# Kernel tuning notes

Hardware: AMD Instinct MI355X
Metric: run time of the kernel (lower is better)

Reference implementation:

```python
import jax, jax.numpy as jnp
import numpy as np

# Mesh hierarchy: V0=20480 -> V1=5120 -> V2=1280 -> V3=320, spiral seq=9, pool nnz/row K=3
B, V0, V1, V2, V3, S, K = 16, 20480, 5120, 1280, 320, 9, 3
CIN, H = 3, (64, 128, 256)
Z = 256


def spiral_conv(x, idx, W, b):
    # x: [B, V_in, C]; idx: [V, S] spiral neighbor indices; W: [S*C, C_out]
    Bx = x.shape[0]
    g = x[:, idx.reshape(-1), :].reshape(Bx, idx.shape[0], -1)  # [B, V, S*C]
    return g @ W + b


def pool(x, idx, w):
    # sparse transform [V_out, V_in] with K nnz per row: idx/w [V_out, K]
    return jnp.einsum('bvkc,vk->bvc', x[:, idx], w)


def setup_inputs() -> dict:
    key = jax.random.key(0)
    ks = iter(jax.random.split(key, 64))

    def nrm(shape, fan_in):
        return jax.random.normal(next(ks), shape, jnp.float32) / np.float32(np.sqrt(fan_in))

    def ridx(shape, hi):
        return jax.random.randint(next(ks), shape, 0, hi, dtype=jnp.int32)

    def pw(shape):
        w = jax.random.uniform(next(ks), shape, jnp.float32)
        return w / jnp.sum(w, axis=-1, keepdims=True)  # row-stochastic pool weights

    inp = {
        'x': jax.random.normal(next(ks), (B, V0, CIN), jnp.float32),
        'enc_W0': nrm((S * CIN, H[0]), S * CIN), 'enc_b0': jnp.zeros((H[0],), jnp.float32),
        'enc_W1': nrm((S * H[0], H[1]), S * H[0]), 'enc_b1': jnp.zeros((H[1],), jnp.float32),
        'enc_W2': nrm((S * H[1], H[2]), S * H[1]), 'enc_b2': jnp.zeros((H[2],), jnp.float32),
        'Wz': nrm((V3 * H[2], Z), V3 * H[2]), 'bz': jnp.zeros((Z,), jnp.float32),
        'Wp': nrm((Z, H[2] * V3), Z), 'bp': jnp.zeros((H[2] * V3,), jnp.float32),
        'dec_W0': nrm((S * H[2], H[1]), S * H[2]), 'dec_b0': jnp.zeros((H[1],), jnp.float32),
        'dec_W1': nrm((S * H[1], H[0]), S * H[1]), 'dec_b1': jnp.zeros((H[0],), jnp.float32),
        'dec_W2': nrm((S * H[0], CIN), S * H[0]), 'dec_b2': jnp.zeros((CIN,), jnp.float32),
        'dpool_w0': pw((V1, K)), 'dpool_w1': pw((V2, K)), 'dpool_w2': pw((V3, K)),
        'upool_w0': pw((V2, K)), 'upool_w1': pw((V1, K)), 'upool_w2': pw((V0, K)),
        'idx0': ridx((V0, S), V0), 'idx1': ridx((V1, S), V1), 'idx2': ridx((V2, S), V2),
        'dpool_idx0': ridx((V1, K), V0), 'dpool_idx1': ridx((V2, K), V1), 'dpool_idx2': ridx((V3, K), V2),
        'upool_idx0': ridx((V2, K), V3), 'upool_idx1': ridx((V1, K), V2), 'upool_idx2': ridx((V0, K), V1),
    }
    return inp


def reference(x, enc_W0, enc_b0, enc_W1, enc_b1, enc_W2, enc_b2, Wz, bz, Wp, bp,
              dec_W0, dec_b0, dec_W1, dec_b1, dec_W2, dec_b2,
              dpool_w0, dpool_w1, dpool_w2, upool_w0, upool_w1, upool_w2,
              idx0, idx1, idx2, dpool_idx0, dpool_idx1, dpool_idx2,
              upool_idx0, upool_idx1, upool_idx2):
    elu = jax.nn.elu
    # ---- encoder: conv -> elu -> down-pool (x3), then flatten -> latent linear
    h = pool(elu(spiral_conv(x, idx0, enc_W0, enc_b0)), dpool_idx0, dpool_w0)   # [B,V1,64]
    h = pool(elu(spiral_conv(h, idx1, enc_W1, enc_b1)), dpool_idx1, dpool_w1)   # [B,V2,128]
    h = pool(elu(spiral_conv(h, idx2, enc_W2, enc_b2)), dpool_idx2, dpool_w2)   # [B,V3,256]
    z = h.reshape(h.shape[0], V3 * H[2]) @ Wz + bz                              # [B,256]
    # ---- decoder: project -> (up-pool -> conv -> act) x3, last act identity
    d = (z @ Wp + bp).reshape(z.shape[0], V3, H[2])                             # [B,V3,256]
    d = elu(spiral_conv(pool(d, upool_idx0, upool_w0), idx2, dec_W0, dec_b0))   # [B,V2,128]
    d = elu(spiral_conv(pool(d, upool_idx1, upool_w1), idx1, dec_W1, dec_b1))   # [B,V1,64]
    y = spiral_conv(pool(d, upool_idx2, upool_w2), idx0, dec_W2, dec_b2)        # [B,V0,3]
    return (y, z)
```

## Files before the change

### kernel.cpp

```cpp
#include <hip/hip_runtime.h>
#include <hip/hip_bf16.h>
#include <math.h>

typedef __hip_bfloat16 bf16;
typedef short bf16x8 __attribute__((ext_vector_type(8)));
typedef float f32x4 __attribute__((ext_vector_type(4)));

__device__ __forceinline__ float bfbits2f(unsigned int u) {
    union { unsigned int i; float f; } c; c.i = u << 16; return c.f;
}
__device__ __forceinline__ float b2f(const bf16 v) {
    return __bfloat162float(v);
}
__device__ __forceinline__ unsigned short f2bbits(float f) {
    unsigned int x = __float_as_uint(f);
    x += 0x7fffu + ((x >> 16) & 1u);
    return (unsigned short)(x >> 16);
}
__device__ __forceinline__ void unpack8(const uint4 v, float* f) {
    f[0]=bfbits2f(v.x & 0xffffu); f[1]=bfbits2f(v.x >> 16);
    f[2]=bfbits2f(v.y & 0xffffu); f[3]=bfbits2f(v.y >> 16);
    f[4]=bfbits2f(v.z & 0xffffu); f[5]=bfbits2f(v.z >> 16);
    f[6]=bfbits2f(v.w & 0xffffu); f[7]=bfbits2f(v.w >> 16);
}
__device__ __forceinline__ float ldx(const float* p) { return *p; }
__device__ __forceinline__ float ldx(const bf16* p)  { return b2f(*p); }

__global__ void zero_k(float* p, int n) {
    int e = blockIdx.x * 256 + threadIdx.x;
    if (e < n) p[e] = 0.f;
}

__global__ void pack_k(const float* __restrict__ W, bf16* __restrict__ o,
                       const int K, const int COUT, const int NT, const int KP32) {
    const int e = blockIdx.x * 256 + threadIdx.x;
    const int total = KP32 * NT * 512;
    if (e >= total) return;
    const int j    = e & 7;
    const int lane = (e >> 3) & 63;
    const int rest = e >> 9;
    const int nt   = rest % NT;
    const int kt2  = rest / NT;
    const int k = kt2 * 32 + ((lane >> 4) << 3) + j;
    const int n = nt * 16 + (lane & 15);
    float v = (k < K && n < COUT) ? W[(size_t)k * COUT + n] : 0.f;
    union { unsigned short u; bf16 h; } c; c.u = f2bbits(v);
    o[e] = c.h;
}

template<typename XT, typename OT, int CIN, int COUT, bool ELU>
__global__ __launch_bounds__(256) void mconv_k(
    const XT* __restrict__ x, const int* __restrict__ idx,
    const bf16* __restrict__ Wpk, const float* __restrict__ bias,
    OT* __restrict__ out, const int V, const int Vin)
{
    constexpr int K    = 9 * CIN;
    constexpr int KC   = (CIN >= 64) ? 64 : 32;
    constexpr int NKC  = (K + KC - 1) / KC;
    constexpr int KS   = KC / 32;
    constexpr int NT   = (COUT + 15) / 16;
    constexpr int ROWB = KC * 2;
    constexpr int SWZ  = (KC == 64) ? 7 : 3;

    __shared__ __align__(16) char alds[2][64 * ROWB];

    const int t  = threadIdx.x;
    const int w  = t >> 6;
    const int l  = t & 63;
    const int r0 = blockIdx.x * 64;
    const int b  = r0 / V;
    const int v0 = r0 - b * V;

    f32x4 acc[NT];
    #pragma unroll
    for (int nt = 0; nt < NT; ++nt) acc[nt] = (f32x4){0.f, 0.f, 0.f, 0.f};

    if constexpr (CIN >= 64) {
        const int srow = t >> 2, u2 = t & 3;
        const int src = idx[(v0 + srow) * 9];
        const XT* gp = x + ((size_t)b * Vin + src) * CIN + u2 * 16;
        const uint4 a0 = *(const uint4*)gp;
        const uint4 a1 = *(const uint4*)(gp + 8);
        char* wb = alds[0] + srow * ROWB;
        const int m = (srow & 7) << 4;
        *(uint4*)(wb + ((u2 * 32) ^ m))      = a0;
        *(uint4*)(wb + ((u2 * 32 + 16) ^ m)) = a1;
    } else {
        for (int e = t; e < 64 * 32; e += 256) {
            const int row = e >> 5, k = e & 31;
            unsigned short hv = 0;
            if (k < K) {
                const int s = k / CIN, ci = k - s * CIN;
                const int src = idx[(v0 + row) * 9 + s];
                hv = f2bbits(ldx(x + ((size_t)b * Vin + src) * CIN + ci));
            }
            const int m2 = (row & 3) << 4;
            *(unsigned short*)(alds[0] + row * 64 + ((k * 2) ^ m2)) = hv;
        }
    }
    __syncthreads();

    const int rl = (w << 4) + (l & 15);
    const int rm = (rl & SWZ) << 4;
    const bf16x8* wpb = (const bf16x8*)Wpk;

    uint4 n0, n1;
    for (int kt = 0; kt < NKC; ++kt) {
        const bool hn = (kt + 1 < NKC);
        if constexpr (CIN >= 64) {
            if (hn) {
                const int srow = t >> 2, u2 = t & 3;
                const int kn = kt + 1;
                const int s   = (kn * 64) / CIN;
                const int ci0 = (kn * 64) - s * CIN;
                const int src = idx[(v0 + srow) * 9 + s];
                const XT* gp = x + ((size_t)b * Vin + src) * CIN + ci0 + u2 * 16;
                n0 = *(const uint4*)gp;
                n1 = *(const uint4*)(gp + 8);
            }
        }
        const char* ab = alds[kt & 1] + rl * ROWB;
        #pragma unroll
        for (int ks = 0; ks < KS; ++ks) {
            union { uint4 u; bf16x8 v; } af;
            af.u = *(const uint4*)(ab + ((ks * 64 + ((l >> 4) << 4)) ^ rm));
            const size_t wbase = ((size_t)(kt * KS + ks) * NT) * 64 + l;
            #pragma unroll
            for (int nt = 0; nt < NT; ++nt) {
                const bf16x8 bfv = wpb[wbase + (size_t)nt * 64];
                acc[nt] = __builtin_amdgcn_mfma_f32_16x16x32_bf16(af.v, bfv, acc[nt], 0, 0, 0);
            }
        }
        if constexpr (CIN >= 64) {
            if (hn) {
                const int srow = t >> 2, u2 = t & 3;
                char* wb = alds[(kt + 1) & 1] + srow * ROWB;
                const int m = (srow & 7) << 4;
                *(uint4*)(wb + ((u2 * 32) ^ m))      = n0;
                *(uint4*)(wb + ((u2 * 32 + 16) ^ m)) = n1;
            }
        }
        __syncthreads();
    }

    const int colg = l & 15;
    const int rg   = (l >> 4) << 2;
    #pragma unroll
    for (int nt = 0; nt < NT; ++nt) {
        const int n = nt * 16 + colg;
        if constexpr (COUT < 16) { if (n >= COUT) continue; }
        const float bv = bias[n];
        #pragma unroll
        for (int rr = 0; rr < 4; ++rr) {
            float a = acc[nt][rr] + bv;
            if constexpr (ELU) a = a > 0.f ? a : (__expf(a) - 1.f);
            const size_t o = (size_t)(r0 + (w << 4) + rg + rr) * COUT + n;
            if constexpr (__is_same(OT, float)) {
                out[o] = a;
            } else {
                union { unsigned short u; bf16 h; } c; c.u = f2bbits(a);
                out[o] = c.h;
            }
        }
    }
}

__global__ __launch_bounds__(256) void pool_k(
    const bf16* __restrict__ in, const int* __restrict__ idx,
    const float* __restrict__ w, bf16* __restrict__ out,
    const int Vout, const int Vin, const int C)
{
    const int nC8 = C >> 3;
    const long long total = (long long)16 * Vout * nC8;
    const long long gid = (long long)blockIdx.x * 256 + threadIdx.x;
    if (gid >= total) return;
    const int c8 = (int)(gid % nC8);
    const long long bv = gid / nC8;
    const int vo = (int)(bv % Vout);
    const int b  = (int)(bv / Vout);

    float r[8];
    #pragma unroll
    for (int u = 0; u < 8; ++u) r[u] = 0.f;
    #pragma unroll
    for (int jj = 0; jj < 3; ++jj) {
        const int src = idx[vo * 3 + jj];
        const float ww = w[vo * 3 + jj];
        const uint4 xv = *(const uint4*)(in + ((size_t)b * Vin + src) * C + c8 * 8);
        float f[8]; unpack8(xv, f);
        #pragma unroll
        for (int u = 0; u < 8; ++u) r[u] += ww * f[u];
    }
    uint4 st;
    st.x = f2bbits(r[0]) | ((unsigned)f2bbits(r[1]) << 16);
    st.y = f2bbits(r[2]) | ((unsigned)f2bbits(r[3]) << 16);
    st.z = f2bbits(r[4]) | ((unsigned)f2bbits(r[5]) << 16);
    st.w = f2bbits(r[6]) | ((unsigned)f2bbits(r[7]) << 16);
    *(uint4*)(out + ((size_t)b * Vout + vo) * C + c8 * 8) = st;
}

__global__ __launch_bounds__(256) void zacc_k(
    const bf16* __restrict__ F, const float* __restrict__ Wz, float* __restrict__ zf)
{
    const int j  = threadIdx.x;
    const int i0 = blockIdx.x * 256;
    float acc[16];
    #pragma unroll
    for (int b = 0; b < 16; ++b) acc[b] = 0.f;
    for (int i = i0; i < i0 + 256; i += 8) {
        float w[8];
        #pragma unroll
        for (int u = 0; u < 8; ++u) w[u] = Wz[(size_t)(i + u) * 256 + j];
        #pragma unroll
        for (int b = 0; b < 16; ++b) {
            const uint4 fv = *(const uint4*)(F + (size_t)b * 81920 + i);
            float f[8]; unpack8(fv, f);
            #pragma unroll
            for (int u = 0; u < 8; ++u) acc[b] += f[u] * w[u];
        }
    }
    #pragma unroll
    for (int b = 0; b < 16; ++b) atomicAdd(&zf[b * 256 + j], acc[b]);
}

__global__ void zfin_k(float* __restrict__ zf, const float* __restrict__ bz,
                       float* __restrict__ outz)
{
    int e = blockIdx.x * 256 + threadIdx.x;
    int j = e & 255;
    float v = zf[e] + bz[j];
    zf[e] = v;
    outz[e] = v;
}

__global__ __launch_bounds__(256) void dproj_k(
    const float* __restrict__ zf, const float* __restrict__ Wp,
    const float* __restrict__ bp, bf16* __restrict__ d)
{
    __shared__ float zl[256][16];
    const int t = threadIdx.x;
    #pragma unroll
    for (int b = 0; b < 16; ++b) zl[t][b] = zf[b * 256 + t];
    __syncthreads();
    const size_t j = (size_t)blockIdx.x * 256 + t;
    const float bpv = bp[j];
    float acc[16];
    #pragma unroll
    for (int b = 0; b < 16; ++b) acc[b] = bpv;
    for (int k = 0; k < 256; ++k) {
        const float w = Wp[(size_t)k * 81920 + j];
        #pragma unroll
        for (int b = 0; b < 16; ++b) acc[b] += zl[k][b] * w;
    }
    #pragma unroll
    for (int b = 0; b < 16; ++b) {
        union { unsigned short u; bf16 h; } c; c.u = f2bbits(acc[b]);
        d[(size_t)b * 81920 + j] = c.h;
    }
}

extern "C" void kernel_launch(void* const* d_in, const int* in_sizes, int n_in,
                              void* d_out, int out_size, void* d_ws, size_t ws_size,
                              hipStream_t stream) {
    (void)in_sizes; (void)n_in; (void)out_size; (void)ws_size;
    const float* x     = (const float*)d_in[0];
    const float* encW0 = (const float*)d_in[1];
    const float* encb0 = (const float*)d_in[2];
    const float* encW1 = (const float*)d_in[3];
    const float* encb1 = (const float*)d_in[4];
    const float* encW2 = (const float*)d_in[5];
    const float* encb2 = (const float*)d_in[6];
    const float* Wz    = (const float*)d_in[7];
    const float* bz    = (const float*)d_in[8];
    const float* Wp    = (const float*)d_in[9];
    const float* bp    = (const float*)d_in[10];
    const float* decW0 = (const float*)d_in[11];
    const float* decb0 = (const float*)d_in[12];
    const float* decW1 = (const float*)d_in[13];
    const float* decb1 = (const float*)d_in[14];
    const float* decW2 = (const float*)d_in[15];
    const float* decb2 = (const float*)d_in[16];
    const float* dpw0  = (const float*)d_in[17];
    const float* dpw1  = (const float*)d_in[18];
    const float* dpw2  = (const float*)d_in[19];
    const float* upw0  = (const float*)d_in[20];
    const float* upw1  = (const float*)d_in[21];
    const float* upw2  = (const float*)d_in[22];
    const int* idx0    = (const int*)d_in[23];
    const int* idx1    = (const int*)d_in[24];
    const int* idx2    = (const int*)d_in[25];
    const int* dpi0    = (const int*)d_in[26];
    const int* dpi1    = (const int*)d_in[27];
    const int* dpi2    = (const int*)d_in[28];
    const int* upi0    = (const int*)d_in[29];
    const int* upi1    = (const int*)d_in[30];
    const int* upi2    = (const int*)d_in[31];

    float* outy = (float*)d_out;
    float* outz = outy + 983040;

    char* ws  = (char*)d_ws;
    float* zf = (float*)ws;
    bf16* P   = (bf16*)(ws + 32768);
    bf16* Q   = P + 20971520;
    bf16* Wbig   = Q + 10485760;
    bf16* dec2pk = P + 10485760;
    bf16* pk_e0 = Wbig;
    bf16* pk_e1 = Wbig + 2048;
    bf16* pk_e2 = Wbig + 75776;
    bf16* pk_d0 = Wbig + 370688;
    bf16* pk_d1 = Wbig + 665600;

    zero_k<<<16, 256, 0, stream>>>(zf, 4096);
    pack_k<<<8,    256, 0, stream>>>(encW0, pk_e0,   27,  64,  4,  1);
    pack_k<<<288,  256, 0, stream>>>(encW1, pk_e1,  576, 128,  8, 18);
    pack_k<<<1152, 256, 0, stream>>>(encW2, pk_e2, 1152, 256, 16, 36);
    pack_k<<<1152, 256, 0, stream>>>(decW0, pk_d0, 2304, 128,  8, 72);
    pack_k<<<288,  256, 0, stream>>>(decW1, pk_d1, 1152,  64,  4, 36);

    mconv_k<float, bf16, 3, 64, true><<<5120, 256, 0, stream>>>(x, idx0, pk_e0, encb0, P, 20480, 20480);
    pool_k<<<2560, 256, 0, stream>>>(P, dpi0, dpw0, Q, 5120, 20480, 64);
    mconv_k<bf16, bf16, 64, 128, true><<<1280, 256, 0, stream>>>(Q, idx1, pk_e1, encb1, P, 5120, 5120);
    pool_k<<<1280, 256, 0, stream>>>(P, dpi1, dpw1, Q, 1280, 5120, 128);
    mconv_k<bf16, bf16, 128, 256, true><<<320, 256, 0, stream>>>(Q, idx2, pk_e2, encb2, P, 1280, 1280);
    pool_k<<<640, 256, 0, stream>>>(P, dpi2, dpw2, Q, 320, 1280, 256);

    zacc_k<<<320, 256, 0, stream>>>(Q, Wz, zf);
    zfin_k<<<16, 256, 0, stream>>>(zf, bz, outz);
    dproj_k<<<320, 256, 0, stream>>>(zf, Wp, bp, P);

    pool_k<<<2560, 256, 0, stream>>>(P, upi0, upw0, Q, 1280, 320, 256);
    mconv_k<bf16, bf16, 256, 128, true><<<320, 256, 0, stream>>>(Q, idx2, pk_d0, decb0, P, 1280, 1280);
    pool_k<<<5120, 256, 0, stream>>>(P, upi1, upw1, Q, 5120, 1280, 128);
    mconv_k<bf16, bf16, 128, 64, true><<<1280, 256, 0, stream>>>(Q, idx1, pk_d1, decb1, P, 5120, 5120);
    pack_k<<<36, 256, 0, stream>>>(decW2, dec2pk, 576, 3, 1, 18);
    pool_k<<<10240, 256, 0, stream>>>(P, upi2, upw2, Q, 20480, 5120, 64);
    mconv_k<bf16, float, 64, 3, false><<<5120, 256, 0, stream>>>(Q, idx0, dec2pk, decb2, outy, 20480, 20480);
}
```

Baseline: 605.9 us.

## Split conv tiles across N warps, prefetch gathers three chunks ahead, specialize first conv

The spiral-conv MFMA kernel gains a WN=2 mode: each block handles 32 rows with two warps splitting the output columns. This doubles the block count for the mid-size layers and raises parallelism. Neighbor indices are loaded into registers once, and gathered activation chunks are prefetched three k-steps ahead through a register ring. One barrier per step feeds a double-buffered LDS tile. The 3-channel first layer gets a dedicated single-MFMA kernel that zero-fills LDS and gathers all 27 inputs at once. The cost is more register pressure from the fully unrolled k-loop and the prefetch buffers, plus duplicated A-tile loads per block.

```diff
diff --git a/kernel.cpp b/kernel.cpp
--- a/kernel.cpp
+++ b/kernel.cpp
@@ -23,8 +23,6 @@
     f[4]=bfbits2f(v.z & 0xffffu); f[5]=bfbits2f(v.z >> 16);
     f[6]=bfbits2f(v.w & 0xffffu); f[7]=bfbits2f(v.w >> 16);
 }
-__device__ __forceinline__ float ldx(const float* p) { return *p; }
-__device__ __forceinline__ float ldx(const bf16* p)  { return b2f(*p); }
 
 __global__ void zero_k(float* p, int n) {
     int e = blockIdx.x * 256 + threadIdx.x;
@@ -48,119 +46,163 @@
     o[e] = c.h;
 }
 
-template<typename XT, typename OT, int CIN, int COUT, bool ELU>
+template<typename OT, int CIN, int COUT, int WN, bool ELU>
 __global__ __launch_bounds__(256) void mconv_k(
-    const XT* __restrict__ x, const int* __restrict__ idx,
+    const bf16* __restrict__ x, const int* __restrict__ idx,
     const bf16* __restrict__ Wpk, const float* __restrict__ bias,
     OT* __restrict__ out, const int V, const int Vin)
 {
     constexpr int K    = 9 * CIN;
-    constexpr int KC   = (CIN >= 64) ? 64 : 32;
-    constexpr int NKC  = (K + KC - 1) / KC;
-    constexpr int KS   = KC / 32;
+    constexpr int NKC  = K / 64;
+    constexpr int KS   = 2;
     constexpr int NT   = (COUT + 15) / 16;
-    constexpr int ROWB = KC * 2;
-    constexpr int SWZ  = (KC == 64) ? 7 : 3;
-
-    __shared__ __align__(16) char alds[2][64 * ROWB];
-
-    const int t  = threadIdx.x;
-    const int w  = t >> 6;
-    const int l  = t & 63;
-    const int r0 = blockIdx.x * 64;
+    constexpr int NTW  = (WN == 2) ? NT / 2 : NT;
+    constexpr int WM   = 4 / WN;
+    constexpr int ROWS = WM * 16;
+    constexpr int LPT  = ROWS / 32;
+    constexpr int PF   = 3;
+
+    __shared__ __align__(16) char alds[2][ROWS * 128];
+
+    const int t = threadIdx.x, w = t >> 6, l = t & 63;
+    const int r0 = blockIdx.x * ROWS;
     const int b  = r0 / V;
     const int v0 = r0 - b * V;
-
-    f32x4 acc[NT];
-    #pragma unroll
-    for (int nt = 0; nt < NT; ++nt) acc[nt] = (f32x4){0.f, 0.f, 0.f, 0.f};
-
-    if constexpr (CIN >= 64) {
-        const int srow = t >> 2, u2 = t & 3;
-        const int src = idx[(v0 + srow) * 9];
-        const XT* gp = x + ((size_t)b * Vin + src) * CIN + u2 * 16;
-        const uint4 a0 = *(const uint4*)gp;
-        const uint4 a1 = *(const uint4*)(gp + 8);
-        char* wb = alds[0] + srow * ROWB;
-        const int m = (srow & 7) << 4;
-        *(uint4*)(wb + ((u2 * 32) ^ m))      = a0;
-        *(uint4*)(wb + ((u2 * 32 + 16) ^ m)) = a1;
-    } else {
-        for (int e = t; e < 64 * 32; e += 256) {
-            const int row = e >> 5, k = e & 31;
-            unsigned short hv = 0;
-            if (k < K) {
-                const int s = k / CIN, ci = k - s * CIN;
-                const int src = idx[(v0 + row) * 9 + s];
-                hv = f2bbits(ldx(x + ((size_t)b * Vin + src) * CIN + ci));
-            }
-            const int m2 = (row & 3) << 4;
-            *(unsigned short*)(alds[0] + row * 64 + ((k * 2) ^ m2)) = hv;
-        }
-    }
-    __syncthreads();
-
-    const int rl = (w << 4) + (l & 15);
-    const int rm = (rl & SWZ) << 4;
+    const size_t bVin = (size_t)b * Vin;
+
+    const int srow = (LPT == 1) ? (t >> 3) : (t >> 2);
+    const int soff = (LPT == 1) ? ((t & 7) << 4) : ((t & 3) << 5);
+    const int smsk = (srow & 7) << 4;
+
+    const int* ip = idx + (v0 + srow) * 9;
+    int nbr[9];
+    #pragma unroll
+    for (int s = 0; s < 9; ++s) nbr[s] = ip[s];
+
+    f32x4 acc[NTW];
+    #pragma unroll
+    for (int nt = 0; nt < NTW; ++nt) acc[nt] = (f32x4){0.f, 0.f, 0.f, 0.f};
+
+    uint4 qa[PF], qb[PF];
+
+    #pragma unroll
+    for (int p = 0; p < PF; ++p) {
+        const int sc = (p * 64) / CIN, cic = (p * 64) % CIN;
+        const bf16* gp = x + (bVin + nbr[sc]) * CIN + cic + (soff >> 1);
+        qa[p] = *(const uint4*)gp;
+        if constexpr (LPT == 2) qb[p] = *(const uint4*)(gp + 8);
+    }
+    {
+        char* wb = alds[0] + srow * 128;
+        *(uint4*)(wb + (soff ^ smsk)) = qa[0];
+        if constexpr (LPT == 2) *(uint4*)(wb + ((soff + 16) ^ smsk)) = qb[0];
+    }
+
+    const int wm = (WN == 2) ? (w >> 1) : w;
+    const int wn = (WN == 2) ? (w & 1) : 0;
+    const int rl = (wm << 4) + (l & 15);
+    const int rm = (rl & 7) << 4;
     const bf16x8* wpb = (const bf16x8*)Wpk;
 
-    uint4 n0, n1;
+    #pragma unroll
     for (int kt = 0; kt < NKC; ++kt) {
-        const bool hn = (kt + 1 < NKC);
-        if constexpr (CIN >= 64) {
-            if (hn) {
-                const int srow = t >> 2, u2 = t & 3;
-                const int kn = kt + 1;
-                const int s   = (kn * 64) / CIN;
-                const int ci0 = (kn * 64) - s * CIN;
-                const int src = idx[(v0 + srow) * 9 + s];
-                const XT* gp = x + ((size_t)b * Vin + src) * CIN + ci0 + u2 * 16;
-                n0 = *(const uint4*)gp;
-                n1 = *(const uint4*)(gp + 8);
-            }
-        }
-        const char* ab = alds[kt & 1] + rl * ROWB;
+        if (kt + PF < NKC) {
+            const int c = kt + PF;
+            const int sc = (c * 64) / CIN, cic = (c * 64) % CIN;
+            const bf16* gp = x + (bVin + nbr[sc]) * CIN + cic + (soff >> 1);
+            qa[c % PF] = *(const uint4*)gp;
+            if constexpr (LPT == 2) qb[c % PF] = *(const uint4*)(gp + 8);
+        }
+        __syncthreads();
+        if (kt + 1 < NKC) {
+            const int p = (kt + 1) % PF;
+            char* wb = alds[(kt + 1) & 1] + srow * 128;
+            *(uint4*)(wb + (soff ^ smsk)) = qa[p];
+            if constexpr (LPT == 2) *(uint4*)(wb + ((soff + 16) ^ smsk)) = qb[p];
+        }
+        const char* ab = alds[kt & 1] + rl * 128;
         #pragma unroll
         for (int ks = 0; ks < KS; ++ks) {
             union { uint4 u; bf16x8 v; } af;
             af.u = *(const uint4*)(ab + ((ks * 64 + ((l >> 4) << 4)) ^ rm));
-            const size_t wbase = ((size_t)(kt * KS + ks) * NT) * 64 + l;
+            const size_t wbase = ((size_t)(kt * KS + ks) * NT + wn * NTW) * 64 + l;
             #pragma unroll
-            for (int nt = 0; nt < NT; ++nt) {
-                const bf16x8 bfv = wpb[wbase + (size_t)nt * 64];
-                acc[nt] = __builtin_amdgcn_mfma_f32_16x16x32_bf16(af.v, bfv, acc[nt], 0, 0, 0);
+            for (int nt = 0; nt < NTW; ++nt) {
+                acc[nt] = __builtin_amdgcn_mfma_f32_16x16x32_bf16(
+                    af.v, wpb[wbase + (size_t)nt * 64], acc[nt], 0, 0, 0);
             }
         }
-        if constexpr (CIN >= 64) {
-            if (hn) {
-                const int srow = t >> 2, u2 = t & 3;
-                char* wb = alds[(kt + 1) & 1] + srow * ROWB;
-                const int m = (srow & 7) << 4;
-                *(uint4*)(wb + ((u2 * 32) ^ m))      = n0;
-                *(uint4*)(wb + ((u2 * 32 + 16) ^ m)) = n1;
-            }
-        }
-        __syncthreads();
     }
 
     const int colg = l & 15;
     const int rg   = (l >> 4) << 2;
     #pragma unroll
-    for (int nt = 0; nt < NT; ++nt) {
-        const int n = nt * 16 + colg;
+    for (int nt = 0; nt < NTW; ++nt) {
+        const int n = (wn * NTW + nt) * 16 + colg;
         if constexpr (COUT < 16) { if (n >= COUT) continue; }
         const float bv = bias[n];
         #pragma unroll
         for (int rr = 0; rr < 4; ++rr) {
             float a = acc[nt][rr] + bv;
             if constexpr (ELU) a = a > 0.f ? a : (__expf(a) - 1.f);
-            const size_t o = (size_t)(r0 + (w << 4) + rg + rr) * COUT + n;
+            const size_t o = (size_t)(r0 + (wm << 4) + rg + rr) * COUT + n;
             if constexpr (__is_same(OT, float)) {
                 out[o] = a;
             } else {
                 union { unsigned short u; bf16 h; } c; c.u = f2bbits(a);
                 out[o] = c.h;
             }
+        }
+    }
+}
+
+__global__ __launch_bounds__(256) void mconv0_k(
+    const float* __restrict__ x, const int* __restrict__ idx,
+    const bf16* __restrict__ Wpk, const float* __restrict__ bias,
+    bf16* __restrict__ out, const int V, const int Vin)
+{
+    __shared__ __align__(16) char alds[64 * 64];
+    const int t = threadIdx.x, w = t >> 6, l = t & 63;
+    const int r0 = blockIdx.x * 64;
+    const int b  = r0 / V;
+    const int v0 = r0 - b * V;
+
+    *(uint4*)(alds + t * 16) = (uint4){0, 0, 0, 0};
+    __syncthreads();
+    for (int e = t; e < 576; e += 256) {
+        const int v = e / 9, s = e - v * 9;
+        const int src = idx[(v0 + v) * 9 + s];
+        const float* gp = x + ((size_t)b * Vin + src) * 3;
+        const int m2 = (v & 3) << 4;
+        char* base = alds + v * 64;
+        #pragma unroll
+        for (int j = 0; j < 3; ++j)
+            *(unsigned short*)(base + (((s * 3 + j) * 2) ^ m2)) = f2bbits(gp[j]);
+    }
+    __syncthreads();
+
+    const int rl = (w << 4) + (l & 15);
+    const int rm = (rl & 3) << 4;
+    union { uint4 u; bf16x8 v; } af;
+    af.u = *(const uint4*)(alds + rl * 64 + ((((l >> 4) << 4)) ^ rm));
+    const bf16x8* wpb = (const bf16x8*)Wpk;
+    f32x4 acc[4];
+    #pragma unroll
+    for (int nt = 0; nt < 4; ++nt) {
+        acc[nt] = (f32x4){0.f, 0.f, 0.f, 0.f};
+        acc[nt] = __builtin_amdgcn_mfma_f32_16x16x32_bf16(af.v, wpb[(size_t)nt * 64 + l], acc[nt], 0, 0, 0);
+    }
+    const int colg = l & 15, rg = (l >> 4) << 2;
+    #pragma unroll
+    for (int nt = 0; nt < 4; ++nt) {
+        const int n = nt * 16 + colg;
+        const float bv = bias[n];
+        #pragma unroll
+        for (int rr = 0; rr < 4; ++rr) {
+            float a = acc[nt][rr] + bv;
+            a = a > 0.f ? a : (__expf(a) - 1.f);
+            union { unsigned short u; bf16 h; } c; c.u = f2bbits(a);
+            out[(size_t)(r0 + (w << 4) + rg + rr) * 64 + n] = c.h;
         }
     }
 }
@@ -318,11 +360,11 @@
     pack_k<<<1152, 256, 0, stream>>>(decW0, pk_d0, 2304, 128,  8, 72);
     pack_k<<<288,  256, 0, stream>>>(decW1, pk_d1, 1152,  64,  4, 36);
 
-    mconv_k<float, bf16, 3, 64, true><<<5120, 256, 0, stream>>>(x, idx0, pk_e0, encb0, P, 20480, 20480);
+    mconv0_k<<<5120, 256, 0, stream>>>(x, idx0, pk_e0, encb0, P, 20480, 20480);
     pool_k<<<2560, 256, 0, stream>>>(P, dpi0, dpw0, Q, 5120, 20480, 64);
-    mconv_k<bf16, bf16, 64, 128, true><<<1280, 256, 0, stream>>>(Q, idx1, pk_e1, encb1, P, 5120, 5120);
+    mconv_k<bf16, 64, 128, 2, true><<<2560, 256, 0, stream>>>(Q, idx1, pk_e1, encb1, P, 5120, 5120);
     pool_k<<<1280, 256, 0, stream>>>(P, dpi1, dpw1, Q, 1280, 5120, 128);
-    mconv_k<bf16, bf16, 128, 256, true><<<320, 256, 0, stream>>>(Q, idx2, pk_e2, encb2, P, 1280, 1280);
+    mconv_k<bf16, 128, 256, 2, true><<<640, 256, 0, stream>>>(Q, idx2, pk_e2, encb2, P, 1280, 1280);
     pool_k<<<640, 256, 0, stream>>>(P, dpi2, dpw2, Q, 320, 1280, 256);
 
     zacc_k<<<320, 256, 0, stream>>>(Q, Wz, zf);
@@ -330,10 +372,10 @@
     dproj_k<<<320, 256, 0, stream>>>(zf, Wp, bp, P);
 
     pool_k<<<2560, 256, 0, stream>>>(P, upi0, upw0, Q, 1280, 320, 256);
-    mconv_k<bf16, bf16, 256, 128, true><<<320, 256, 0, stream>>>(Q, idx2, pk_d0, decb0, P, 1280, 1280);
+    mconv_k<bf16, 256, 128, 2, true><<<640, 256, 0, stream>>>(Q, idx2, pk_d0, decb0, P, 1280, 1280);
     pool_k<<<5120, 256, 0, stream>>>(P, upi1, upw1, Q, 5120, 1280, 128);
-    mconv_k<bf16, bf16, 128, 64, true><<<1280, 256, 0, stream>>>(Q, idx1, pk_d1, decb1, P, 5120, 5120);
+    mconv_k<bf16, 128, 64, 2, true><<<2560, 256, 0, stream>>>(Q, idx1, pk_d1, decb1, P, 5120, 5120);
     pack_k<<<36, 256, 0, stream>>>(decW2, dec2pk, 576, 3, 1, 18);
     pool_k<<<10240, 256, 0, stream>>>(P, upi2, upw2, Q, 20480, 5120, 64);
-    mconv_k<bf16, float, 64, 3, false><<<5120, 256, 0, stream>>>(Q, idx0, dec2pk, decb2, outy, 20480, 20480);
-}
+    mconv_k<float, 64, 3, 1, false><<<5120, 256, 0, stream>>>(Q, idx0, dec2pk, decb2, outy, 20480, 20480);
+}
```

New measurement: 727.4 us. +20.1%, slower.
